# Kernel optimization log

Measured on AMD Instinct MI355X. Metric: run time of the kernel, lower is better.

Reference implementation:

```python
import jax, jax.numpy as jnp
import numpy as np

B, T, S, L, D, H = 2, 1024, 8, 256, 1024, 16
DH = D // H
EPS = 1e-5


def layer_norm(x, w, b):
    m = jnp.mean(x, axis=-1, keepdims=True)
    v = jnp.mean(jnp.square(x - m), axis=-1, keepdims=True)
    return (x - m) * jax.lax.rsqrt(v + EPS) * w + b


def setup_inputs() -> dict:
    key = jax.random.key(0)
    ks = jax.random.split(key, 12)
    s = 0.02
    return {
        "target_hidden": jax.random.normal(ks[0], (B, T, D), jnp.float32),
        "support_hidden": jax.random.normal(ks[1], (B, S, L, D), jnp.float32),
        "support_features": jax.random.normal(ks[2], (B, T, 3), jnp.float32),
        "support_token_mask": jax.random.randint(ks[3], (B, S, L), 0, 2).astype(bool),
        "ln_q_w": jnp.ones((D,), jnp.float32), "ln_q_b": jnp.zeros((D,), jnp.float32),
        "ln_kv_w": jnp.ones((D,), jnp.float32), "ln_kv_b": jnp.zeros((D,), jnp.float32),
        "out_ln_w": jnp.ones((D,), jnp.float32), "out_ln_b": jnp.zeros((D,), jnp.float32),
        "in_proj_w": jax.random.normal(ks[4], (3 * D, D), jnp.float32) * s,
        "in_proj_b": jnp.zeros((3 * D,), jnp.float32),
        "out_proj_w": jax.random.normal(ks[5], (D, D), jnp.float32) * s,
        "out_proj_b": jnp.zeros((D,), jnp.float32),
        "gate_w1": jax.random.normal(ks[6], (D, 2 * D + 3), jnp.float32) * s,
        "gate_b1": jnp.zeros((D,), jnp.float32),
        "gate_w2": jax.random.normal(ks[7], (1, D), jnp.float32) * s,
        "gate_b2": jnp.zeros((1,), jnp.float32),
    }


def _forward(target_hidden, support_hidden, support_features,
             ln_q_w, ln_q_b, ln_kv_w, ln_kv_b, out_ln_w, out_ln_b,
             in_proj_w, in_proj_b, out_proj_w, out_proj_b,
             gate_w1, gate_b1, gate_w2, gate_b2, support_token_mask):
    b, ns, sl, d = support_hidden.shape
    kv_len = ns * sl
    support_flat = support_hidden.reshape(b, kv_len, d)
    mask_flat = support_token_mask.reshape(b, kv_len)  # True = valid token

    q_in = layer_norm(target_hidden, ln_q_w, ln_q_b)
    kv_in = layer_norm(support_flat, ln_kv_w, ln_kv_b)

    # in-projection (torch MHA packed qkv weight)
    q = q_in @ in_proj_w[:d].T + in_proj_b[:d]
    k = kv_in @ in_proj_w[d:2 * d].T + in_proj_b[d:2 * d]
    v = kv_in @ in_proj_w[2 * d:].T + in_proj_b[2 * d:]

    qh = q.reshape(b, -1, H, DH)
    kh = k.reshape(b, kv_len, H, DH)
    vh = v.reshape(b, kv_len, H, DH)

    scores = jnp.einsum("bthd,bshd->bhts", qh, kh) / jnp.sqrt(jnp.float32(DH))
    scores = jnp.where(mask_flat[:, None, None, :], scores, -jnp.inf)
    probs = jax.nn.softmax(scores, axis=-1)
    ctx = jnp.einsum("bhts,bshd->bthd", probs, vh).reshape(b, -1, d)
    attn_out = ctx @ out_proj_w.T + out_proj_b

    gate_in = jnp.concatenate([target_hidden, attn_out, support_features], axis=-1)
    h = jax.nn.gelu(gate_in @ gate_w1.T + gate_b1, approximate=False)
    gate = jax.nn.sigmoid(h @ gate_w2.T + gate_b2)  # [b, t, 1]

    fused = gate * attn_out + (1.0 - gate) * target_hidden
    out = layer_norm(target_hidden + fused, out_ln_w, out_ln_b)
    return out, gate.squeeze(-1)


def reference(target_hidden, support_hidden, support_features, support_token_mask,
              ln_q_w, ln_q_b, ln_kv_w, ln_kv_b, out_ln_w, out_ln_b,
              in_proj_w, in_proj_b, out_proj_w, out_proj_b,
              gate_w1, gate_b1, gate_w2, gate_b2):
    return _forward(target_hidden, support_hidden, support_features,
                    ln_q_w, ln_q_b, ln_kv_w, ln_kv_b, out_ln_w, out_ln_b,
                    in_proj_w, in_proj_b, out_proj_w, out_proj_b,
                    gate_w1, gate_b1, gate_w2, gate_b2, support_token_mask)
```

## Files before the change

kernel.cpp:

```cpp
#include <hip/hip_runtime.h>
#include <stdint.h>

#define DEV __device__ __forceinline__

typedef __attribute__((ext_vector_type(8))) short bf16x8;
typedef __attribute__((ext_vector_type(4))) float f32x4;

DEV unsigned short f2bf(float f) {
  unsigned u = __float_as_uint(f);
  return (unsigned short)((u + 0x7fffu + ((u >> 16) & 1u)) >> 16);
}
DEV float bf2f(unsigned short h) { return __uint_as_float(((unsigned)h) << 16); }

DEV void async16(const void* g, void* l) {
  __builtin_amdgcn_global_load_lds((const __attribute__((address_space(1))) void*)g,
                                   (__attribute__((address_space(3))) void*)l, 16, 0, 0);
}

__global__ void k_cvt4(const float4* __restrict__ s, ushort4* __restrict__ d, int n4) {
  int i = blockIdx.x * 256 + threadIdx.x;
  if (i < n4) {
    float4 v = s[i];
    ushort4 o;
    o.x = f2bf(v.x); o.y = f2bf(v.y); o.z = f2bf(v.z); o.w = f2bf(v.w);
    d[i] = o;
  }
}

__global__ void k_cvt_pad(const float* __restrict__ s, unsigned short* __restrict__ d,
                          int rows, int sc, int dc) {
  int n = rows * dc;
  for (int i = blockIdx.x * 256 + threadIdx.x; i < n; i += gridDim.x * 256) {
    int r = i / dc, c = i - r * dc;
    d[i] = (c < sc) ? f2bf(s[(size_t)r * sc + c]) : (unsigned short)0;
  }
}

__global__ void k_mask_build(const unsigned char* __restrict__ m, float* __restrict__ mf) {
  int any = 0;
  for (int i = threadIdx.x; i < 4096; i += 256)
    if ((i & 3) != 0 && m[i] != 0) any = 1;
  unsigned long long ball = __ballot(any);
  __shared__ int sr[4];
  if ((threadIdx.x & 63) == 0) sr[threadIdx.x >> 6] = (ball != 0ULL) ? 1 : 0;
  __syncthreads();
  int isbool = sr[0] | sr[1] | sr[2] | sr[3];
  int i = blockIdx.x * 256 + threadIdx.x;
  if (i < 4096) {
    int v = isbool ? (m[i] != 0) : (((const int*)m)[i] != 0);
    mf[i] = v ? -8.0f : -1e30f;
  }
}

__global__ void k_ln(const float* __restrict__ x, const float* __restrict__ w,
                     const float* __restrict__ b, unsigned short* __restrict__ y) {
  int row = blockIdx.x;
  float4 v = ((const float4*)(x + (size_t)row * 1024))[threadIdx.x];
  float s = v.x + v.y + v.z + v.w;
  float ss = v.x * v.x + v.y * v.y + v.z * v.z + v.w * v.w;
#pragma unroll
  for (int m = 32; m >= 1; m >>= 1) { s += __shfl_xor(s, m); ss += __shfl_xor(ss, m); }
  __shared__ float red[8];
  int wv = threadIdx.x >> 6;
  if ((threadIdx.x & 63) == 0) { red[wv] = s; red[4 + wv] = ss; }
  __syncthreads();
  s = red[0] + red[1] + red[2] + red[3];
  ss = red[4] + red[5] + red[6] + red[7];
  float mean = s * (1.f / 1024.f);
  float var = ss * (1.f / 1024.f) - mean * mean;
  float inv = rsqrtf(var + 1e-5f);
  float4 wv4 = ((const float4*)w)[threadIdx.x];
  float4 bv4 = ((const float4*)b)[threadIdx.x];
  ushort4 o;
  o.x = f2bf((v.x - mean) * inv * wv4.x + bv4.x);
  o.y = f2bf((v.y - mean) * inv * wv4.y + bv4.y);
  o.z = f2bf((v.z - mean) * inv * wv4.z + bv4.z);
  o.w = f2bf((v.w - mean) * inv * wv4.w + bv4.w);
  ((ushort4*)(y + (size_t)row * 1024))[threadIdx.x] = o;
}

template <int BM, int BN, int OUTMODE>
DEV void gemm_body(const unsigned short* __restrict__ A, const unsigned short* __restrict__ B,
                   const float* __restrict__ bias, void* __restrict__ Cout, int N, int K,
                   int m0, int n0, float* __restrict__ aux) {
  constexpr int WM = BM / 2, WN = BN / 2, FM = WM / 16, FN = WN / 16;
  __shared__ __align__(16) unsigned short As[2][BM * 32];
  __shared__ __align__(16) unsigned short Bs[2][BN * 32];
  int tid = threadIdx.x, l = tid & 63, w = tid >> 6;
  int wm = w >> 1, wn = w & 1;

  f32x4 acc[FM][FN];
#pragma unroll
  for (int m = 0; m < FM; m++)
#pragma unroll
    for (int n = 0; n < FN; n++) acc[m][n] = (f32x4){0.f, 0.f, 0.f, 0.f};

  auto stage = [&](int buf, int k0) {
#pragma unroll
    for (int i = 0; i < BM / 64; i++) {
      int r = i * 64 + w * 16 + (l >> 2);
      int cb = ((l & 3) * 16) ^ (((r >> 1) & 3) << 4);
      async16((const char*)A + (((size_t)(m0 + r) * K + k0) * 2 + cb),
              (char*)&As[buf][0] + (i * 64 + w * 16) * 64);
    }
#pragma unroll
    for (int i = 0; i < BN / 64; i++) {
      int r = i * 64 + w * 16 + (l >> 2);
      int cb = ((l & 3) * 16) ^ (((r >> 1) & 3) << 4);
      async16((const char*)B + (((size_t)(n0 + r) * K + k0) * 2 + cb),
              (char*)&Bs[buf][0] + (i * 64 + w * 16) * 64);
    }
  };

  int nk = K / 32;
  stage(0, 0);
  __syncthreads();
  int cur = 0;
  for (int kt = 0; kt < nk; kt++) {
    if (kt + 1 < nk) stage(cur ^ 1, (kt + 1) * 32);
    bf16x8 af[FM], bfr[FN];
#pragma unroll
    for (int m = 0; m < FM; m++) {
      int rr = wm * WM + m * 16 + (l & 15);
      af[m] = *(const bf16x8*)((const char*)&As[cur][0] + rr * 64 +
                               ((16 * (l >> 4)) ^ (((rr >> 1) & 3) << 4)));
    }
#pragma unroll
    for (int n = 0; n < FN; n++) {
      int rr = wn * WN + n * 16 + (l & 15);
      bfr[n] = *(const bf16x8*)((const char*)&Bs[cur][0] + rr * 64 +
                                ((16 * (l >> 4)) ^ (((rr >> 1) & 3) << 4)));
    }
    __builtin_amdgcn_s_setprio(1);
#pragma unroll
    for (int m = 0; m < FM; m++)
#pragma unroll
      for (int n = 0; n < FN; n++)
        acc[m][n] = __builtin_amdgcn_mfma_f32_16x16x32_bf16(af[m], bfr[n], acc[m][n], 0, 0, 0);
    __builtin_amdgcn_s_setprio(0);
    __syncthreads();
    cur ^= 1;
  }

#pragma unroll
  for (int m = 0; m < FM; m++)
#pragma unroll
    for (int n = 0; n < FN; n++)
#pragma unroll
      for (int r = 0; r < 4; r++) {
        int gr = m0 + wm * WM + m * 16 + (l >> 4) * 4 + r;
        int gc = n0 + wn * WN + n * 16 + (l & 15);
        float v = acc[m][n][r] + bias[gc];
        if (OUTMODE == 2) v = 0.5f * v * (1.f + erff(v * 0.70710678118f));
        if (OUTMODE == 3) {
          aux[(size_t)gr * 1024 + gc] = v;
          ((unsigned short*)Cout)[(size_t)gr * 2080 + 1024 + gc] = f2bf(v);
        } else {
          ((unsigned short*)Cout)[(size_t)gr * N + gc] = f2bf(v);
        }
      }
}

template <int BM, int BN, int OUTMODE>
__global__ __launch_bounds__(256, 2)
void k_gemm(const unsigned short* __restrict__ A, const unsigned short* __restrict__ B,
            const float* __restrict__ bias, void* __restrict__ Cout, int N, int K,
            int nx, float* __restrict__ aux) {
  int cpx = gridDim.x >> 3;
  int orig = (blockIdx.x & 7) * cpx + (blockIdx.x >> 3);
  int m0 = (orig / nx) * BM, n0 = (orig % nx) * BN;
  gemm_body<BM, BN, OUTMODE>(A, B, bias, Cout, N, K, m0, n0, aux);
}

__global__ __launch_bounds__(256, 2)
void k_inproj(const unsigned short* __restrict__ qin, const unsigned short* __restrict__ kvin,
              const unsigned short* __restrict__ Wbf, const float* __restrict__ ipb,
              unsigned short* __restrict__ qbuf, unsigned short* __restrict__ kvbuf) {
  int cpx = gridDim.x >> 3;
  int orig = (blockIdx.x & 7) * cpx + (blockIdx.x >> 3);
  if (orig < 128) {
    int m0 = (orig >> 3) * 128, n0 = (orig & 7) * 128;
    gemm_body<128, 128, 0>(qin, Wbf, ipb, qbuf, 1024, 1024, m0, n0, nullptr);
  } else {
    int t = orig - 128;
    int m0 = (t >> 4) * 128, n0 = (t & 15) * 128;
    gemm_body<128, 128, 0>(kvin, Wbf + 1024 * 1024, ipb + 1024, kvbuf, 2048, 1024, m0, n0,
                           nullptr);
  }
}

__global__ void k_transpose_v(const unsigned short* __restrict__ kvb,
                              unsigned short* __restrict__ vt) {
  __shared__ unsigned short t[64][66];
  int kv0 = blockIdx.x * 64, d0 = blockIdx.y * 64, b = blockIdx.z;
  for (int i = threadIdx.x; i < 4096; i += 256) {
    int r = i >> 6, c = i & 63;
    t[r][c] = kvb[(size_t)(b * 2048 + kv0 + r) * 2048 + 1024 + d0 + c];
  }
  __syncthreads();
  for (int i = threadIdx.x; i < 4096; i += 256) {
    int r = i >> 6, c = i & 63;
    vt[(size_t)(b * 1024 + d0 + r) * 2048 + kv0 + c] = t[c][r];
  }
}

__global__ __launch_bounds__(256, 2)
void k_attn(const unsigned short* __restrict__ qb, const unsigned short* __restrict__ kvb,
            const unsigned short* __restrict__ vt, const float* __restrict__ mf,
            unsigned short* __restrict__ po, float* __restrict__ plsum) {
  __shared__ __align__(16) unsigned short Kt[2][64 * 64];
  __shared__ __align__(16) unsigned short Vs[2][64 * 64];
  __shared__ __align__(16) unsigned short Pl[4][16 * 64];
  int tid = threadIdx.x, l = tid & 63, w = tid >> 6;
  int id = blockIdx.x;
  int hb = id & 31, half = (id >> 5) & 1, qt = id >> 6;
  int h = hb & 15, b = hb >> 4;
  int q0 = qt * 64 + w * 16;
  int kvbase = half * 1024;

  const char* qsrc = (const char*)qb +
      ((size_t)(b * 1024 + q0 + (l & 15)) * 1024 + h * 64 + 8 * (l >> 4)) * 2;
  bf16x8 aq0 = *(const bf16x8*)qsrc;
  bf16x8 aq1 = *(const bf16x8*)(qsrc + 64);

  const char* kbase = (const char*)kvb + ((size_t)(b * 2048) * 2048 + h * 64) * 2;
  const char* vbase = (const char*)vt + ((size_t)(b * 1024 + h * 64) * 2048) * 2;
  const float* mrow = mf + b * 2048;

  f32x4 oacc[4], osum;
#pragma unroll
  for (int dt = 0; dt < 4; dt++) oacc[dt] = (f32x4){0.f, 0.f, 0.f, 0.f};
  osum = (f32x4){0.f, 0.f, 0.f, 0.f};

  bf16x8 onesf;
#pragma unroll
  for (int e = 0; e < 8; e++) onesf[e] = ((l & 15) == 0) ? (short)0x3F80 : (short)0;

  auto stage = [&](int buf, int kvabs) {
#pragma unroll
    for (int i = 0; i < 2; i++) {
      int r = i * 32 + w * 8 + (l >> 3);
      int cb = ((l & 7) * 16) ^ ((r & 7) << 4);
      async16(kbase + (size_t)(kvabs + r) * 4096 + cb, (char*)&Kt[buf][0] + (i * 32 + w * 8) * 128);
      async16(vbase + (size_t)r * 4096 + (size_t)kvabs * 2 + cb,
              (char*)&Vs[buf][0] + (i * 32 + w * 8) * 128);
    }
  };

  stage(0, kvbase);
  __syncthreads();
  int cur = 0;

  for (int t = 0; t < 16; t++) {
    int kvabs = kvbase + t * 64;
    if (t < 15) stage(cur ^ 1, kvabs + 64);

    float mcol[4];
#pragma unroll
    for (int st = 0; st < 4; st++) mcol[st] = mrow[kvabs + st * 16 + (l & 15)];

    f32x4 sacc[4];
#pragma unroll
    for (int st = 0; st < 4; st++) sacc[st] = (f32x4){0.f, 0.f, 0.f, 0.f};
    const char* kt = (const char*)&Kt[cur][0];
    __builtin_amdgcn_s_setprio(1);
#pragma unroll
    for (int st = 0; st < 4; st++) {
      int rr = st * 16 + (l & 15);
      bf16x8 bk0 = *(const bf16x8*)(kt + rr * 128 + ((16 * (l >> 4)) ^ ((rr & 7) << 4)));
      bf16x8 bk1 = *(const bf16x8*)(kt + rr * 128 + ((64 + 16 * (l >> 4)) ^ ((rr & 7) << 4)));
      sacc[st] = __builtin_amdgcn_mfma_f32_16x16x32_bf16(aq0, bk0, sacc[st], 0, 0, 0);
      sacc[st] = __builtin_amdgcn_mfma_f32_16x16x32_bf16(aq1, bk1, sacc[st], 0, 0, 0);
    }
    __builtin_amdgcn_s_setprio(0);

#pragma unroll
    for (int r = 0; r < 4; r++) {
      int q = (l >> 4) * 4 + r;
      unsigned xm = (q & 7) << 4;
      char* pb = (char*)(&Pl[w][0]) + q * 128;
#pragma unroll
      for (int st = 0; st < 4; st++) {
        float p = __expf(fmaf(sacc[st][r], 0.125f, mcol[st]));
        *(unsigned short*)(pb + ((((l & 15) * 2) + st * 32) ^ xm)) = f2bf(p);
      }
    }

    const char* vsb = (const char*)&Vs[cur][0];
    __builtin_amdgcn_s_setprio(1);
#pragma unroll
    for (int ch = 0; ch < 2; ch++) {
      int q2 = l & 15;
      bf16x8 pa = *(const bf16x8*)((const char*)(&Pl[w][0]) + q2 * 128 +
                                   ((ch * 64 + 16 * (l >> 4)) ^ ((q2 & 7) << 4)));
#pragma unroll
      for (int dt = 0; dt < 4; dt++) {
        int dr = dt * 16 + (l & 15);
        bf16x8 bv = *(const bf16x8*)(vsb + dr * 128 +
                                     ((ch * 64 + 16 * (l >> 4)) ^ ((dr & 7) << 4)));
        oacc[dt] = __builtin_amdgcn_mfma_f32_16x16x32_bf16(pa, bv, oacc[dt], 0, 0, 0);
      }
      osum = __builtin_amdgcn_mfma_f32_16x16x32_bf16(pa, onesf, osum, 0, 0, 0);
    }
    __builtin_amdgcn_s_setprio(0);
    __syncthreads();
    cur ^= 1;
  }

#pragma unroll
  for (int dt = 0; dt < 4; dt++)
#pragma unroll
    for (int r = 0; r < 4; r++) {
      size_t gr = (size_t)half * 2048 + b * 1024 + q0 + (l >> 4) * 4 + r;
      po[gr * 1024 + h * 64 + dt * 16 + (l & 15)] = f2bf(oacc[dt][r]);
    }
  if ((l & 15) == 0) {
#pragma unroll
    for (int r = 0; r < 4; r++) {
      size_t gr = (size_t)half * 2048 + b * 1024 + q0 + (l >> 4) * 4 + r;
      plsum[gr * 16 + h] = osum[r];
    }
  }
}

__global__ void k_combine(const unsigned short* __restrict__ po, const float* __restrict__ plsum,
                          unsigned short* __restrict__ ctx) {
  int row = blockIdx.x, t = threadIdx.x;
  int head = t >> 4;
  float inv = 1.f / (plsum[(size_t)row * 16 + head] + plsum[(size_t)(2048 + row) * 16 + head]);
  ushort4 a = ((const ushort4*)(po + (size_t)row * 1024))[t];
  ushort4 c = ((const ushort4*)(po + (size_t)(2048 + row) * 1024))[t];
  ushort4 o;
  o.x = f2bf((bf2f(a.x) + bf2f(c.x)) * inv);
  o.y = f2bf((bf2f(a.y) + bf2f(c.y)) * inv);
  o.z = f2bf((bf2f(a.z) + bf2f(c.z)) * inv);
  o.w = f2bf((bf2f(a.w) + bf2f(c.w)) * inv);
  ((ushort4*)(ctx + (size_t)row * 1024))[t] = o;
}

__global__ void k_gin_static(const float* __restrict__ target, const float* __restrict__ feats,
                             unsigned short* __restrict__ gi) {
  int i = blockIdx.x * 256 + threadIdx.x;
  const int ntgt = 2048 * 1024;
  if (i < ntgt) {
    int r = i >> 10, c = i & 1023;
    gi[(size_t)r * 2080 + c] = f2bf(target[i]);
  } else {
    int j = i - ntgt;
    if (j < 2048 * 32) {
      int r = j >> 5, c = j & 31;
      gi[(size_t)r * 2080 + 2048 + c] = (c < 3) ? f2bf(feats[r * 3 + c]) : (unsigned short)0;
    }
  }
}

__global__ void k_gatefinal(const unsigned short* __restrict__ hm, const float* __restrict__ w2,
                            const float* __restrict__ b2, const float* __restrict__ target,
                            const float* __restrict__ attn, const float* __restrict__ w,
                            const float* __restrict__ bb, float* __restrict__ out,
                            float* __restrict__ gout) {
  int row = blockIdx.x;
  float4 w2v = ((const float4*)w2)[threadIdx.x];
  ushort4 hv = ((const ushort4*)(hm + (size_t)row * 1024))[threadIdx.x];
  float s = bf2f(hv.x) * w2v.x + bf2f(hv.y) * w2v.y + bf2f(hv.z) * w2v.z + bf2f(hv.w) * w2v.w;
#pragma unroll
  for (int m = 32; m >= 1; m >>= 1) s += __shfl_xor(s, m);
  __shared__ float red[8];
  __shared__ float gsh;
  if ((threadIdx.x & 63) == 0) red[threadIdx.x >> 6] = s;
  __syncthreads();
  if (threadIdx.x == 0) {
    float tt = red[0] + red[1] + red[2] + red[3] + b2[0];
    float gv = 1.f / (1.f + __expf(-tt));
    gsh = gv;
    gout[row] = gv;
  }
  __syncthreads();
  float gv = gsh;

  float4 t = ((const float4*)(target + (size_t)row * 1024))[threadIdx.x];
  float4 a = ((const float4*)(attn + (size_t)row * 1024))[threadIdx.x];
  float4 y;
  y.x = (2.f - gv) * t.x + gv * a.x;
  y.y = (2.f - gv) * t.y + gv * a.y;
  y.z = (2.f - gv) * t.z + gv * a.z;
  y.w = (2.f - gv) * t.w + gv * a.w;
  float sm = y.x + y.y + y.z + y.w;
  float ss = y.x * y.x + y.y * y.y + y.z * y.z + y.w * y.w;
#pragma unroll
  for (int m = 32; m >= 1; m >>= 1) { sm += __shfl_xor(sm, m); ss += __shfl_xor(ss, m); }
  if ((threadIdx.x & 63) == 0) { red[threadIdx.x >> 6] = sm; red[4 + (threadIdx.x >> 6)] = ss; }
  __syncthreads();
  sm = red[0] + red[1] + red[2] + red[3];
  ss = red[4] + red[5] + red[6] + red[7];
  float mean = sm * (1.f / 1024.f);
  float var = ss * (1.f / 1024.f) - mean * mean;
  float inv = rsqrtf(var + 1e-5f);
  float4 wv4 = ((const float4*)w)[threadIdx.x];
  float4 bv4 = ((const float4*)bb)[threadIdx.x];
  float4 o;
  o.x = (y.x - mean) * inv * wv4.x + bv4.x;
  o.y = (y.y - mean) * inv * wv4.y + bv4.y;
  o.z = (y.z - mean) * inv * wv4.z + bv4.z;
  o.w = (y.w - mean) * inv * wv4.w + bv4.w;
  ((float4*)(out + (size_t)row * 1024))[threadIdx.x] = o;
}

extern "C" void kernel_launch(void* const* d_in, const int* in_sizes, int n_in,
                              void* d_out, int out_size, void* d_ws, size_t ws_size,
                              hipStream_t stream) {
  const float* target     = (const float*)d_in[0];
  const float* support    = (const float*)d_in[1];
  const float* feats      = (const float*)d_in[2];
  const void*  maskp      = d_in[3];
  const float* ln_q_w     = (const float*)d_in[4];
  const float* ln_q_b     = (const float*)d_in[5];
  const float* ln_kv_w    = (const float*)d_in[6];
  const float* ln_kv_b    = (const float*)d_in[7];
  const float* out_ln_w   = (const float*)d_in[8];
  const float* out_ln_b   = (const float*)d_in[9];
  const float* in_proj_w  = (const float*)d_in[10];
  const float* in_proj_b  = (const float*)d_in[11];
  const float* out_proj_w = (const float*)d_in[12];
  const float* out_proj_b = (const float*)d_in[13];
  const float* gate_w1    = (const float*)d_in[14];
  const float* gate_b1    = (const float*)d_in[15];
  const float* gate_w2    = (const float*)d_in[16];
  const float* gate_b2    = (const float*)d_in[17];

  if (ws_size < 67330052ULL) return;

  char* ws = (char*)d_ws;
  unsigned short* Wbf   = (unsigned short*)(ws + 0);
  unsigned short* Wobf  = (unsigned short*)(ws + 6291456);
  unsigned short* Wg1bf = (unsigned short*)(ws + 8388608);
  unsigned short* qin   = (unsigned short*)(ws + 12648448);
  unsigned short* kvin  = (unsigned short*)(ws + 16842752);
  unsigned short* qbuf  = (unsigned short*)(ws + 25231360);
  unsigned short* kvbuf = (unsigned short*)(ws + 29425664);
  unsigned short* vtbuf = (unsigned short*)(ws + 12648448);
  float*          plsum = (float*)(ws + 21037056);
  unsigned short* hbuf  = (unsigned short*)(ws + 21299200);
  unsigned short* ctx   = (unsigned short*)(ws + 46202880);
  unsigned short* po    = (unsigned short*)(ws + 50397184);
  float*          attn  = (float*)(ws + 50397184);
  unsigned short* gin   = (unsigned short*)(ws + 58785792);
  float*          maskf = (float*)(ws + 67313664);

  float* outp = (float*)d_out;

  k_mask_build<<<16, 256, 0, stream>>>((const unsigned char*)maskp, maskf);

  k_cvt4<<<3072, 256, 0, stream>>>((const float4*)in_proj_w, (ushort4*)Wbf, 3072 * 256);
  k_cvt4<<<1024, 256, 0, stream>>>((const float4*)out_proj_w, (ushort4*)Wobf, 1024 * 256);
  k_cvt_pad<<<2048, 256, 0, stream>>>(gate_w1, Wg1bf, 1024, 2051, 2080);
  k_gin_static<<<(2048 * 1056 + 255) / 256, 256, 0, stream>>>(target, feats, gin);

  k_ln<<<2048, 256, 0, stream>>>(target, ln_q_w, ln_q_b, qin);
  k_ln<<<4096, 256, 0, stream>>>(support, ln_kv_w, ln_kv_b, kvin);

  k_inproj<<<640, 256, 0, stream>>>(qin, kvin, Wbf, in_proj_b, qbuf, kvbuf);

  k_transpose_v<<<dim3(32, 16, 2), 256, 0, stream>>>(kvbuf, vtbuf);

  k_attn<<<1024, 256, 0, stream>>>(qbuf, kvbuf, vtbuf, maskf, po, plsum);
  k_combine<<<2048, 256, 0, stream>>>(po, plsum, ctx);

  k_gemm<64, 64, 3><<<512, 256, 0, stream>>>(ctx, Wobf, out_proj_b, gin, 1024, 1024, 16, attn);

  k_gemm<64, 64, 2><<<512, 256, 0, stream>>>(gin, Wg1bf, gate_b1, hbuf, 1024, 2080, 16, nullptr);

  k_gatefinal<<<2048, 256, 0, stream>>>(hbuf, gate_w2, gate_b2, target, attn,
                                        out_ln_w, out_ln_b, outp, outp + 2 * 1024 * 1024);
}
```

Before: 276.7 us.

## Rewrite attention with 32x32 MFMA, register-resident P, four-way KV split

Attention moves from 16x16x32 to 32x32x16 MFMA with a transposed formulation (K and V as the A operand, Q and P as the B operand), which removes the LDS round-trip for P by using cvt_pk_bf16 and permlane32_swap. The mask is added through an extra MFMA against a ones vector, and the softmax scale is folded into the Q projection epilogue. The KV range is split into four segments instead of two, with transposed partial outputs and a new combine kernel. Weight-conversion launches and the two layer-norm launches are also merged to cut launch count. The trade-off is more partial-output traffic and a larger workspace, plus bf16 rounding of the mask and scale values.

```diff
diff --git a/kernel.cpp b/kernel.cpp
--- a/kernel.cpp
+++ b/kernel.cpp
@@ -5,6 +5,8 @@
 
 typedef __attribute__((ext_vector_type(8))) short bf16x8;
 typedef __attribute__((ext_vector_type(4))) float f32x4;
+typedef __attribute__((ext_vector_type(16))) float f32x16;
+typedef __attribute__((ext_vector_type(8))) unsigned short ushort8;
 
 DEV unsigned short f2bf(float f) {
   unsigned u = __float_as_uint(f);
@@ -12,31 +14,43 @@
 }
 DEV float bf2f(unsigned short h) { return __uint_as_float(((unsigned)h) << 16); }
 
+DEV unsigned cvtpk(float lo, float hi) {
+  unsigned r;
+  asm("v_cvt_pk_bf16_f32 %0, %1, %2" : "=v"(r) : "v"(lo), "v"(hi));
+  return r;
+}
+DEV void pl32swap(unsigned& a, unsigned& b) {
+  asm volatile("v_permlane32_swap_b32 %0, %1" : "+v"(a), "+v"(b));
+}
+
 DEV void async16(const void* g, void* l) {
   __builtin_amdgcn_global_load_lds((const __attribute__((address_space(1))) void*)g,
                                    (__attribute__((address_space(3))) void*)l, 16, 0, 0);
 }
 
-__global__ void k_cvt4(const float4* __restrict__ s, ushort4* __restrict__ d, int n4) {
-  int i = blockIdx.x * 256 + threadIdx.x;
-  if (i < n4) {
-    float4 v = s[i];
-    ushort4 o;
-    o.x = f2bf(v.x); o.y = f2bf(v.y); o.z = f2bf(v.z); o.w = f2bf(v.w);
-    d[i] = o;
-  }
-}
-
-__global__ void k_cvt_pad(const float* __restrict__ s, unsigned short* __restrict__ d,
-                          int rows, int sc, int dc) {
-  int n = rows * dc;
-  for (int i = blockIdx.x * 256 + threadIdx.x; i < n; i += gridDim.x * 256) {
-    int r = i / dc, c = i - r * dc;
-    d[i] = (c < sc) ? f2bf(s[(size_t)r * sc + c]) : (unsigned short)0;
-  }
-}
-
-__global__ void k_mask_build(const unsigned char* __restrict__ m, float* __restrict__ mf) {
+__global__ void k_prep(const float4* __restrict__ ipw, const float4* __restrict__ opw,
+                       const float* __restrict__ g1w, ushort4* __restrict__ Wbf,
+                       ushort4* __restrict__ Wobf, unsigned short* __restrict__ Wg1bf) {
+  int bid = blockIdx.x, t = threadIdx.x;
+  if (bid < 3072) {
+    int i = bid * 256 + t;
+    float4 v = ipw[i];
+    ushort4 o; o.x = f2bf(v.x); o.y = f2bf(v.y); o.z = f2bf(v.z); o.w = f2bf(v.w);
+    Wbf[i] = o;
+  } else if (bid < 4096) {
+    int i = (bid - 3072) * 256 + t;
+    float4 v = opw[i];
+    ushort4 o; o.x = f2bf(v.x); o.y = f2bf(v.y); o.z = f2bf(v.z); o.w = f2bf(v.w);
+    Wobf[i] = o;
+  } else {
+    for (int i = (bid - 4096) * 256 + t; i < 1024 * 2080; i += 2048 * 256) {
+      int r = i / 2080, c = i - r * 2080;
+      Wg1bf[i] = (c < 2051) ? f2bf(g1w[(size_t)r * 2051 + c]) : (unsigned short)0;
+    }
+  }
+}
+
+__global__ void k_mask_build(const unsigned char* __restrict__ m, unsigned short* __restrict__ mf) {
   int any = 0;
   for (int i = threadIdx.x; i < 4096; i += 256)
     if ((i & 3) != 0 && m[i] != 0) any = 1;
@@ -48,14 +62,20 @@
   int i = blockIdx.x * 256 + threadIdx.x;
   if (i < 4096) {
     int v = isbool ? (m[i] != 0) : (((const int*)m)[i] != 0);
-    mf[i] = v ? -8.0f : -1e30f;
-  }
-}
-
-__global__ void k_ln(const float* __restrict__ x, const float* __restrict__ w,
-                     const float* __restrict__ b, unsigned short* __restrict__ y) {
+    mf[i] = v ? f2bf(-8.0f) : f2bf(-1e30f);
+  }
+}
+
+__global__ void k_ln2(const float* __restrict__ tgt, const float* __restrict__ sup,
+                      const float* __restrict__ qw, const float* __restrict__ qb,
+                      const float* __restrict__ kw, const float* __restrict__ kb,
+                      unsigned short* __restrict__ qin, unsigned short* __restrict__ kvin) {
   int row = blockIdx.x;
-  float4 v = ((const float4*)(x + (size_t)row * 1024))[threadIdx.x];
+  const float *x, *w, *bb;
+  unsigned short* y;
+  if (row < 2048) { x = tgt + (size_t)row * 1024; w = qw; bb = qb; y = qin + (size_t)row * 1024; }
+  else { int r = row - 2048; x = sup + (size_t)r * 1024; w = kw; bb = kb; y = kvin + (size_t)r * 1024; }
+  float4 v = ((const float4*)x)[threadIdx.x];
   float s = v.x + v.y + v.z + v.w;
   float ss = v.x * v.x + v.y * v.y + v.z * v.z + v.w * v.w;
 #pragma unroll
@@ -70,19 +90,19 @@
   float var = ss * (1.f / 1024.f) - mean * mean;
   float inv = rsqrtf(var + 1e-5f);
   float4 wv4 = ((const float4*)w)[threadIdx.x];
-  float4 bv4 = ((const float4*)b)[threadIdx.x];
+  float4 bv4 = ((const float4*)bb)[threadIdx.x];
   ushort4 o;
   o.x = f2bf((v.x - mean) * inv * wv4.x + bv4.x);
   o.y = f2bf((v.y - mean) * inv * wv4.y + bv4.y);
   o.z = f2bf((v.z - mean) * inv * wv4.z + bv4.z);
   o.w = f2bf((v.w - mean) * inv * wv4.w + bv4.w);
-  ((ushort4*)(y + (size_t)row * 1024))[threadIdx.x] = o;
+  ((ushort4*)y)[threadIdx.x] = o;
 }
 
 template <int BM, int BN, int OUTMODE>
 DEV void gemm_body(const unsigned short* __restrict__ A, const unsigned short* __restrict__ B,
                    const float* __restrict__ bias, void* __restrict__ Cout, int N, int K,
-                   int m0, int n0, float* __restrict__ aux) {
+                   int m0, int n0, float* __restrict__ aux, float oscale) {
   constexpr int WM = BM / 2, WN = BN / 2, FM = WM / 16, FN = WN / 16;
   __shared__ __align__(16) unsigned short As[2][BM * 32];
   __shared__ __align__(16) unsigned short Bs[2][BN * 32];
@@ -150,7 +170,7 @@
       for (int r = 0; r < 4; r++) {
         int gr = m0 + wm * WM + m * 16 + (l >> 4) * 4 + r;
         int gc = n0 + wn * WN + n * 16 + (l & 15);
-        float v = acc[m][n][r] + bias[gc];
+        float v = (acc[m][n][r] + bias[gc]) * oscale;
         if (OUTMODE == 2) v = 0.5f * v * (1.f + erff(v * 0.70710678118f));
         if (OUTMODE == 3) {
           aux[(size_t)gr * 1024 + gc] = v;
@@ -169,7 +189,7 @@
   int cpx = gridDim.x >> 3;
   int orig = (blockIdx.x & 7) * cpx + (blockIdx.x >> 3);
   int m0 = (orig / nx) * BM, n0 = (orig % nx) * BN;
-  gemm_body<BM, BN, OUTMODE>(A, B, bias, Cout, N, K, m0, n0, aux);
+  gemm_body<BM, BN, OUTMODE>(A, B, bias, Cout, N, K, m0, n0, aux, 1.0f);
 }
 
 __global__ __launch_bounds__(256, 2)
@@ -180,12 +200,12 @@
   int orig = (blockIdx.x & 7) * cpx + (blockIdx.x >> 3);
   if (orig < 128) {
     int m0 = (orig >> 3) * 128, n0 = (orig & 7) * 128;
-    gemm_body<128, 128, 0>(qin, Wbf, ipb, qbuf, 1024, 1024, m0, n0, nullptr);
+    gemm_body<128, 128, 0>(qin, Wbf, ipb, qbuf, 1024, 1024, m0, n0, nullptr, 0.125f);
   } else {
     int t = orig - 128;
     int m0 = (t >> 4) * 128, n0 = (t & 15) * 128;
     gemm_body<128, 128, 0>(kvin, Wbf + 1024 * 1024, ipb + 1024, kvbuf, 2048, 1024, m0, n0,
-                           nullptr);
+                           nullptr, 1.0f);
   }
 }
 
@@ -206,136 +226,156 @@
 
 __global__ __launch_bounds__(256, 2)
 void k_attn(const unsigned short* __restrict__ qb, const unsigned short* __restrict__ kvb,
-            const unsigned short* __restrict__ vt, const float* __restrict__ mf,
-            unsigned short* __restrict__ po, float* __restrict__ plsum) {
-  __shared__ __align__(16) unsigned short Kt[2][64 * 64];
-  __shared__ __align__(16) unsigned short Vs[2][64 * 64];
-  __shared__ __align__(16) unsigned short Pl[4][16 * 64];
+            const unsigned short* __restrict__ vt, const unsigned short* __restrict__ maskbf,
+            unsigned short* __restrict__ pot, float* __restrict__ plsum) {
+  __shared__ __align__(16) unsigned short Kt[2][32 * 64];
+  __shared__ __align__(16) unsigned short Vt[2][64 * 32];
+  __shared__ __align__(16) unsigned short mls[512];
   int tid = threadIdx.x, l = tid & 63, w = tid >> 6;
+  int hi = l >> 5, q32 = l & 31;
   int id = blockIdx.x;
-  int hb = id & 31, half = (id >> 5) & 1, qt = id >> 6;
+  int hb = id & 31, rest = id >> 5;
+  int qt = rest >> 2, seg = rest & 3;
   int h = hb & 15, b = hb >> 4;
-  int q0 = qt * 64 + w * 16;
-  int kvbase = half * 1024;
-
-  const char* qsrc = (const char*)qb +
-      ((size_t)(b * 1024 + q0 + (l & 15)) * 1024 + h * 64 + 8 * (l >> 4)) * 2;
-  bf16x8 aq0 = *(const bf16x8*)qsrc;
-  bf16x8 aq1 = *(const bf16x8*)(qsrc + 64);
-
-  const char* kbase = (const char*)kvb + ((size_t)(b * 2048) * 2048 + h * 64) * 2;
-  const char* vbase = (const char*)vt + ((size_t)(b * 1024 + h * 64) * 2048) * 2;
-  const float* mrow = mf + b * 2048;
-
-  f32x4 oacc[4], osum;
-#pragma unroll
-  for (int dt = 0; dt < 4; dt++) oacc[dt] = (f32x4){0.f, 0.f, 0.f, 0.f};
-  osum = (f32x4){0.f, 0.f, 0.f, 0.f};
-
-  bf16x8 onesf;
-#pragma unroll
-  for (int e = 0; e < 8; e++) onesf[e] = ((l & 15) == 0) ? (short)0x3F80 : (short)0;
-
-  auto stage = [&](int buf, int kvabs) {
-#pragma unroll
-    for (int i = 0; i < 2; i++) {
-      int r = i * 32 + w * 8 + (l >> 3);
-      int cb = ((l & 7) * 16) ^ ((r & 7) << 4);
-      async16(kbase + (size_t)(kvabs + r) * 4096 + cb, (char*)&Kt[buf][0] + (i * 32 + w * 8) * 128);
-      async16(vbase + (size_t)r * 4096 + (size_t)kvabs * 2 + cb,
-              (char*)&Vs[buf][0] + (i * 32 + w * 8) * 128);
-    }
+  int qrow = qt * 128 + w * 32 + q32;
+  int kv0base = seg * 512;
+
+  bf16x8 fq[4];
+  const char* qsrc = (const char*)qb + (((size_t)(b * 1024 + qrow)) * 1024 + h * 64 + hi * 8) * 2;
+#pragma unroll
+  for (int i = 0; i < 4; i++) fq[i] = *(const bf16x8*)(qsrc + i * 32);
+
+  bf16x8 onesB = {0, 0, 0, 0, 0, 0, 0, 0};
+  if (hi == 0) onesB[0] = (short)0x3F80;
+
+  f32x16 oa0 = {0, 0, 0, 0, 0, 0, 0, 0, 0, 0, 0, 0, 0, 0, 0, 0};
+  f32x16 oa1 = {0, 0, 0, 0, 0, 0, 0, 0, 0, 0, 0, 0, 0, 0, 0, 0};
+  float plocal = 0.f;
+
+  if (w == 0)
+    async16((const char*)maskbf + ((size_t)b * 2048 + kv0base) * 2 + l * 16, (char*)mls);
+
+  const char* kgb = (const char*)kvb + ((size_t)(b * 2048)) * 4096 + h * 128;
+  const char* vgb = (const char*)vt + ((size_t)(b * 1024 + h * 64)) * 4096;
+  int kcb = (((l & 7) ^ ((l >> 3) & 7)) << 4);
+  int vcb = (((l & 3) ^ ((l >> 3) & 3)) << 4);
+
+  auto stage = [&](int buf, int kv0) {
+    async16(kgb + (size_t)(kv0 + w * 8 + (l >> 3)) * 4096 + kcb, (char*)&Kt[buf][0] + w * 1024);
+    async16(vgb + (size_t)(w * 16 + (l >> 2)) * 4096 + (size_t)kv0 * 2 + vcb,
+            (char*)&Vt[buf][0] + w * 1024);
   };
 
-  stage(0, kvbase);
+  stage(0, kv0base);
   __syncthreads();
   int cur = 0;
 
+  int kfs = q32 & 7;
+  int vfs = (q32 >> 1) & 3;
+
   for (int t = 0; t < 16; t++) {
-    int kvabs = kvbase + t * 64;
-    if (t < 15) stage(cur ^ 1, kvabs + 64);
-
-    float mcol[4];
-#pragma unroll
-    for (int st = 0; st < 4; st++) mcol[st] = mrow[kvabs + st * 16 + (l & 15)];
-
-    f32x4 sacc[4];
-#pragma unroll
-    for (int st = 0; st < 4; st++) sacc[st] = (f32x4){0.f, 0.f, 0.f, 0.f};
+    int kv0 = kv0base + t * 32;
+    if (t < 15) stage(cur ^ 1, kv0 + 32);
+
+    f32x16 sac = {0, 0, 0, 0, 0, 0, 0, 0, 0, 0, 0, 0, 0, 0, 0, 0};
     const char* kt = (const char*)&Kt[cur][0];
     __builtin_amdgcn_s_setprio(1);
 #pragma unroll
-    for (int st = 0; st < 4; st++) {
-      int rr = st * 16 + (l & 15);
-      bf16x8 bk0 = *(const bf16x8*)(kt + rr * 128 + ((16 * (l >> 4)) ^ ((rr & 7) << 4)));
-      bf16x8 bk1 = *(const bf16x8*)(kt + rr * 128 + ((64 + 16 * (l >> 4)) ^ ((rr & 7) << 4)));
-      sacc[st] = __builtin_amdgcn_mfma_f32_16x16x32_bf16(aq0, bk0, sacc[st], 0, 0, 0);
-      sacc[st] = __builtin_amdgcn_mfma_f32_16x16x32_bf16(aq1, bk1, sacc[st], 0, 0, 0);
-    }
+    for (int i = 0; i < 4; i++) {
+      bf16x8 ka = *(const bf16x8*)(kt + q32 * 128 + (((i * 2 + hi) ^ kfs) << 4));
+      sac = __builtin_amdgcn_mfma_f32_32x32x16_bf16(ka, fq[i], sac, 0, 0, 0);
+    }
+    unsigned short mv = mls[t * 32 + q32];
+    bf16x8 ma = {0, 0, 0, 0, 0, 0, 0, 0};
+    if (hi == 0) ma[0] = (short)mv;
+    sac = __builtin_amdgcn_mfma_f32_32x32x16_bf16(ma, onesB, sac, 0, 0, 0);
     __builtin_amdgcn_s_setprio(0);
 
-#pragma unroll
-    for (int r = 0; r < 4; r++) {
-      int q = (l >> 4) * 4 + r;
-      unsigned xm = (q & 7) << 4;
-      char* pb = (char*)(&Pl[w][0]) + q * 128;
-#pragma unroll
-      for (int st = 0; st < 4; st++) {
-        float p = __expf(fmaf(sacc[st][r], 0.125f, mcol[st]));
-        *(unsigned short*)(pb + ((((l & 15) * 2) + st * 32) ^ xm)) = f2bf(p);
-      }
-    }
-
-    const char* vsb = (const char*)&Vs[cur][0];
+    float p[16];
+#pragma unroll
+    for (int j = 0; j < 16; j++) p[j] = __expf(sac[j]);
+#pragma unroll
+    for (int j = 0; j < 16; j++) plocal += p[j];
+
+    bf16x8 pf[2];
+#pragma unroll
+    for (int c = 0; c < 2; c++) {
+      unsigned A0 = cvtpk(p[c * 8 + 0], p[c * 8 + 1]);
+      unsigned A1 = cvtpk(p[c * 8 + 2], p[c * 8 + 3]);
+      unsigned B0 = cvtpk(p[c * 8 + 4], p[c * 8 + 5]);
+      unsigned B1 = cvtpk(p[c * 8 + 6], p[c * 8 + 7]);
+      pl32swap(A0, B0);
+      pl32swap(A1, B1);
+      unsigned fr[4] = {A0, A1, B0, B1};
+      pf[c] = *(const bf16x8*)fr;
+    }
+
+    const char* vtb = (const char*)&Vt[cur][0];
     __builtin_amdgcn_s_setprio(1);
 #pragma unroll
-    for (int ch = 0; ch < 2; ch++) {
-      int q2 = l & 15;
-      bf16x8 pa = *(const bf16x8*)((const char*)(&Pl[w][0]) + q2 * 128 +
-                                   ((ch * 64 + 16 * (l >> 4)) ^ ((q2 & 7) << 4)));
-#pragma unroll
-      for (int dt = 0; dt < 4; dt++) {
-        int dr = dt * 16 + (l & 15);
-        bf16x8 bv = *(const bf16x8*)(vsb + dr * 128 +
-                                     ((ch * 64 + 16 * (l >> 4)) ^ ((dr & 7) << 4)));
-        oacc[dt] = __builtin_amdgcn_mfma_f32_16x16x32_bf16(pa, bv, oacc[dt], 0, 0, 0);
-      }
-      osum = __builtin_amdgcn_mfma_f32_16x16x32_bf16(pa, onesf, osum, 0, 0, 0);
+    for (int c = 0; c < 2; c++) {
+      bf16x8 va0 = *(const bf16x8*)(vtb + q32 * 64 + (((c * 2 + hi) ^ vfs) << 4));
+      bf16x8 va1 = *(const bf16x8*)(vtb + (32 + q32) * 64 + (((c * 2 + hi) ^ vfs) << 4));
+      oa0 = __builtin_amdgcn_mfma_f32_32x32x16_bf16(va0, pf[c], oa0, 0, 0, 0);
+      oa1 = __builtin_amdgcn_mfma_f32_32x32x16_bf16(va1, pf[c], oa1, 0, 0, 0);
     }
     __builtin_amdgcn_s_setprio(0);
     __syncthreads();
     cur ^= 1;
   }
 
-#pragma unroll
-  for (int dt = 0; dt < 4; dt++)
-#pragma unroll
-    for (int r = 0; r < 4; r++) {
-      size_t gr = (size_t)half * 2048 + b * 1024 + q0 + (l >> 4) * 4 + r;
-      po[gr * 1024 + h * 64 + dt * 16 + (l & 15)] = f2bf(oacc[dt][r]);
-    }
-  if ((l & 15) == 0) {
-#pragma unroll
-    for (int r = 0; r < 4; r++) {
-      size_t gr = (size_t)half * 2048 + b * 1024 + q0 + (l >> 4) * 4 + r;
-      plsum[gr * 16 + h] = osum[r];
-    }
-  }
-}
-
-__global__ void k_combine(const unsigned short* __restrict__ po, const float* __restrict__ plsum,
-                          unsigned short* __restrict__ ctx) {
-  int row = blockIdx.x, t = threadIdx.x;
-  int head = t >> 4;
-  float inv = 1.f / (plsum[(size_t)row * 16 + head] + plsum[(size_t)(2048 + row) * 16 + head]);
-  ushort4 a = ((const ushort4*)(po + (size_t)row * 1024))[t];
-  ushort4 c = ((const ushort4*)(po + (size_t)(2048 + row) * 1024))[t];
-  ushort4 o;
-  o.x = f2bf((bf2f(a.x) + bf2f(c.x)) * inv);
-  o.y = f2bf((bf2f(a.y) + bf2f(c.y)) * inv);
-  o.z = f2bf((bf2f(a.z) + bf2f(c.z)) * inv);
-  o.w = f2bf((bf2f(a.w) + bf2f(c.w)) * inv);
-  ((ushort4*)(ctx + (size_t)row * 1024))[t] = o;
+  float ptot = plocal + __shfl_xor(plocal, 32);
+  if (hi == 0) plsum[((size_t)seg * 2048 + b * 1024 + qrow) * 16 + h] = ptot;
+
+  size_t pb = (((size_t)seg * 2 + b) * 16 + h) * 64;
+#pragma unroll
+  for (int j = 0; j < 16; j++) {
+    int d0 = (j & 3) + 8 * (j >> 2) + 4 * hi;
+    pot[(pb + d0) * 1024 + qrow] = f2bf(oa0[j]);
+    pot[(pb + 32 + d0) * 1024 + qrow] = f2bf(oa1[j]);
+  }
+}
+
+__global__ void k_combine_t(const unsigned short* __restrict__ pot,
+                            const float* __restrict__ plsum, unsigned short* __restrict__ ctx) {
+  __shared__ float sinv[64];
+  __shared__ __align__(16) unsigned short tl[64][72];
+  int t = threadIdx.x;
+  int id = blockIdx.x;
+  int qt2 = id & 15, bh = id >> 4, h = bh & 15, b = bh >> 4;
+  int q0 = qt2 * 64;
+
+  if (t < 64) {
+    float s = 0.f;
+#pragma unroll
+    for (int seg = 0; seg < 4; seg++)
+      s += plsum[((size_t)seg * 2048 + b * 1024 + q0 + t) * 16 + h];
+    sinv[t] = 1.f / s;
+  }
+
+  int d = t >> 2, qo = (t & 3) * 16;
+  float acc[16];
+#pragma unroll
+  for (int j = 0; j < 16; j++) acc[j] = 0.f;
+#pragma unroll
+  for (int seg = 0; seg < 4; seg++) {
+    size_t base = ((((size_t)seg * 2 + b) * 16 + h) * 64 + d) * 1024 + q0 + qo;
+    ushort8 v0 = *(const ushort8*)(pot + base);
+    ushort8 v1 = *(const ushort8*)(pot + base + 8);
+#pragma unroll
+    for (int j = 0; j < 8; j++) { acc[j] += bf2f(v0[j]); acc[8 + j] += bf2f(v1[j]); }
+  }
+  __syncthreads();
+#pragma unroll
+  for (int j = 0; j < 16; j++) tl[qo + j][d] = f2bf(acc[j] * sinv[qo + j]);
+  __syncthreads();
+
+  int q = t >> 2, dof = (t & 3) * 16;
+  ushort8 a = *(const ushort8*)&tl[q][dof];
+  ushort8 c8 = *(const ushort8*)&tl[q][dof + 8];
+  size_t ob = ((size_t)(b * 1024 + q0 + q)) * 1024 + h * 64 + dof;
+  *(ushort8*)(ctx + ob) = a;
+  *(ushort8*)(ctx + ob + 8) = c8;
 }
 
 __global__ void k_gin_static(const float* __restrict__ target, const float* __restrict__ feats,
@@ -428,43 +468,38 @@
   const float* gate_w2    = (const float*)d_in[16];
   const float* gate_b2    = (const float*)d_in[17];
 
-  if (ws_size < 67330052ULL) return;
+  if (ws_size < 84615168ULL) return;
 
   char* ws = (char*)d_ws;
-  unsigned short* Wbf   = (unsigned short*)(ws + 0);
-  unsigned short* Wobf  = (unsigned short*)(ws + 6291456);
-  unsigned short* Wg1bf = (unsigned short*)(ws + 8388608);
-  unsigned short* qin   = (unsigned short*)(ws + 12648448);
-  unsigned short* kvin  = (unsigned short*)(ws + 16842752);
-  unsigned short* qbuf  = (unsigned short*)(ws + 25231360);
-  unsigned short* kvbuf = (unsigned short*)(ws + 29425664);
-  unsigned short* vtbuf = (unsigned short*)(ws + 12648448);
-  float*          plsum = (float*)(ws + 21037056);
-  unsigned short* hbuf  = (unsigned short*)(ws + 21299200);
-  unsigned short* ctx   = (unsigned short*)(ws + 46202880);
-  unsigned short* po    = (unsigned short*)(ws + 50397184);
-  float*          attn  = (float*)(ws + 50397184);
-  unsigned short* gin   = (unsigned short*)(ws + 58785792);
-  float*          maskf = (float*)(ws + 67313664);
+  unsigned short* Wbf    = (unsigned short*)(ws + 0);
+  unsigned short* Wobf   = (unsigned short*)(ws + 6291456);
+  unsigned short* Wg1bf  = (unsigned short*)(ws + 8388608);
+  unsigned short* qin    = (unsigned short*)(ws + 12648448);
+  unsigned short* kvin   = (unsigned short*)(ws + 16842752);
+  unsigned short* qbuf   = (unsigned short*)(ws + 25231360);
+  unsigned short* kvbuf  = (unsigned short*)(ws + 29425664);
+  unsigned short* vtbuf  = (unsigned short*)(ws + 12648448);
+  unsigned short* hbuf   = (unsigned short*)(ws + 25231360);
+  unsigned short* ctx    = (unsigned short*)(ws + 46202880);
+  float*          attn   = (float*)(ws + 50397184);
+  unsigned short* gin    = (unsigned short*)(ws + 58785792);
+  unsigned short* pot    = (unsigned short*)(ws + 67305472);
+  float*          plsum  = (float*)(ws + 84082688);
+  unsigned short* maskbf = (unsigned short*)(ws + 84606976);
 
   float* outp = (float*)d_out;
 
-  k_mask_build<<<16, 256, 0, stream>>>((const unsigned char*)maskp, maskf);
-
-  k_cvt4<<<3072, 256, 0, stream>>>((const float4*)in_proj_w, (ushort4*)Wbf, 3072 * 256);
-  k_cvt4<<<1024, 256, 0, stream>>>((const float4*)out_proj_w, (ushort4*)Wobf, 1024 * 256);
-  k_cvt_pad<<<2048, 256, 0, stream>>>(gate_w1, Wg1bf, 1024, 2051, 2080);
+  k_mask_build<<<16, 256, 0, stream>>>((const unsigned char*)maskp, maskbf);
+  k_prep<<<6144, 256, 0, stream>>>((const float4*)in_proj_w, (const float4*)out_proj_w,
+                                   gate_w1, (ushort4*)Wbf, (ushort4*)Wobf, Wg1bf);
   k_gin_static<<<(2048 * 1056 + 255) / 256, 256, 0, stream>>>(target, feats, gin);
-
-  k_ln<<<2048, 256, 0, stream>>>(target, ln_q_w, ln_q_b, qin);
-  k_ln<<<4096, 256, 0, stream>>>(support, ln_kv_w, ln_kv_b, kvin);
+  k_ln2<<<6144, 256, 0, stream>>>(target, support, ln_q_w, ln_q_b, ln_kv_w, ln_kv_b, qin, kvin);
 
   k_inproj<<<640, 256, 0, stream>>>(qin, kvin, Wbf, in_proj_b, qbuf, kvbuf);
-
   k_transpose_v<<<dim3(32, 16, 2), 256, 0, stream>>>(kvbuf, vtbuf);
 
-  k_attn<<<1024, 256, 0, stream>>>(qbuf, kvbuf, vtbuf, maskf, po, plsum);
-  k_combine<<<2048, 256, 0, stream>>>(po, plsum, ctx);
+  k_attn<<<1024, 256, 0, stream>>>(qbuf, kvbuf, vtbuf, maskbf, pot, plsum);
+  k_combine_t<<<512, 256, 0, stream>>>(pot, plsum, ctx);
 
   k_gemm<64, 64, 3><<<512, 256, 0, stream>>>(ctx, Wobf, out_proj_b, gin, 1024, 1024, 16, attn);
 
```

Result: faster. 265.9 us (-3.9%).
